# Kernel optimization log

Measured on AMD Instinct MI355X. Metric: run time of the kernel, lower is better.

The kernel has to match this reference:

```python
import jax, jax.numpy as jnp
import numpy as np

K_TOP = 4          # self.k
NUM_EXPERTS = 16   # self.num_experts
LOSS_COEF = 0.01


def setup_inputs() -> dict:
    key = jax.random.key(0)
    k0, k1, k2, k3, k4 = jax.random.split(key, 5)
    B, Cin, Cout, H, Wd, E = 16, 64, 64, 64, 64, NUM_EXPERTS
    x = jax.random.normal(k0, (B, Cin, H, Wd), dtype=jnp.float32)
    w_gate = jax.random.normal(k1, (Cin, E), dtype=jnp.float32) * 0.1
    w_noise = jax.random.normal(k2, (Cin, E), dtype=jnp.float32) * 0.1
    W = jax.random.normal(k3, (E, Cout, Cin, 3, 3), dtype=jnp.float32) * (1.0 / np.sqrt(Cin * 9).astype(np.float32))
    b = jax.random.normal(k4, (E, Cout), dtype=jnp.float32) * 0.01
    return {"x": x, "w_gate": w_gate, "w_noise": w_noise, "W": W, "b": b, "train": 0}


def _cv_squared(v):
    # torch .var() is unbiased (ddof=1)
    v = v.astype(jnp.float32)
    return jnp.var(v, ddof=1) / (jnp.mean(v) ** 2 + 1e-10)


def reference(x, w_gate, w_noise, W, b, train):
    B = x.shape[0]
    E = NUM_EXPERTS
    # gate_x = flatten(avgpool(x)) -> [B, Cin]
    gate_x = jnp.mean(x, axis=(2, 3))
    clean_logits = gate_x @ w_gate                      # [B, E]
    # train == 0 (eval): no noise branch; logits = softmax(clean_logits)
    logits = jax.nn.softmax(clean_logits, axis=1)
    top_vals, top_idx = jax.lax.top_k(logits, min(K_TOP + 1, E))
    tk_vals = top_vals[:, :K_TOP]                       # [B, k]
    tk_idx = top_idx[:, :K_TOP]                         # [B, k]
    tk_gates = tk_vals / (jnp.sum(tk_vals, axis=1, keepdims=True) + 1e-6)
    gates = jnp.zeros_like(logits).at[jnp.arange(B)[:, None], tk_idx].set(tk_gates)  # [B, E]
    # load (eval path): count of nonzero gates per expert
    load = jax.lax.stop_gradient(jnp.sum(gates > 0, axis=0)).astype(jnp.float32)     # [E]
    importance = jnp.sum(gates, axis=0)                 # [E]
    loss = (_cv_squared(importance) + _cv_squared(load)) * LOSS_COEF
    # dispatch/combine == dense gated mixture: zero-gate experts contribute 0.
    def conv_one(w):
        return jax.lax.conv_general_dilated(
            x, w, window_strides=(1, 1), padding=[(1, 1), (1, 1)],
            dimension_numbers=("NCHW", "OIHW", "NCHW"))
    expert_outs = jax.vmap(conv_one)(W) + b[:, None, :, None, None]  # [E, B, Cout, H, W]
    y = jnp.einsum("ebchw,be->bchw", expert_outs, gates)
    return (y, loss)
```

## Files before the change

### kernel.cpp

```cpp
#include <hip/hip_runtime.h>
#include <hip/hip_bf16.h>


typedef __attribute__((ext_vector_type(8))) short bf16x8;
typedef __attribute__((ext_vector_type(4))) float f32x4;

__device__ inline unsigned short f2bf(float f) {
  unsigned u = __builtin_bit_cast(unsigned, f);
  unsigned r = u + 0x7FFFu + ((u >> 16) & 1u);
  return (unsigned short)(r >> 16);
}

__global__ __launch_bounds__(256) void transpose_kernel(const float* __restrict__ x,
                                                        unsigned short* __restrict__ xt,
                                                        float* __restrict__ gpart) {
  int bh = blockIdx.x;
  int b = bh >> 6, h = bh & 63;
  __shared__ float tile[64][65];
  int t = threadIdx.x;
  int w = t & 63, c0 = t >> 6;
#pragma unroll
  for (int i = 0; i < 16; ++i) {
    int ci = c0 * 16 + i;
    tile[ci][w] = x[(((size_t)b * 64 + ci) * 64 + h) * 64 + w];
  }
  __syncthreads();
  if (t < 64) {
    float s = 0.f;
#pragma unroll
    for (int w2 = 0; w2 < 64; ++w2) s += tile[t][w2];
    gpart[(size_t)bh * 64 + t] = s;
  }
#pragma unroll
  for (int it = 0; it < 2; ++it) {
    int idx = t + it * 256;
    int g = idx >> 6;
    int wo = idx & 63;
    bf16x8 v;
#pragma unroll
    for (int j = 0; j < 8; ++j) v[j] = (short)f2bf(tile[g * 8 + j][wo]);
    *(bf16x8*)(xt + (((size_t)bh * 8 + g) * 64 + wo) * 8) = v;
  }
}

__global__ __launch_bounds__(256) void gate_kernel(const float* __restrict__ gpart,
                                                   const float* __restrict__ w_gate,
                                                   float* __restrict__ tkg,
                                                   int* __restrict__ tki,
                                                   float* __restrict__ loss_out) {
  __shared__ float red[4][64];
  __shared__ float sgx[16][64];
  __shared__ float sl[16][16];
  __shared__ float sg[16][16];
  __shared__ float simp[16], sld[16];
  int t = threadIdx.x;
  int hg = t >> 6, ci = t & 63;
  for (int b = 0; b < 16; ++b) {
    float s = 0.f;
#pragma unroll
    for (int hh = 0; hh < 16; ++hh)
      s += gpart[((size_t)(b * 64 + hg * 16 + hh)) * 64 + ci];
    red[hg][ci] = s;
    __syncthreads();
    if (t < 64) sgx[b][t] = (red[0][t] + red[1][t] + red[2][t] + red[3][t]) * (1.0f / 4096.0f);
    __syncthreads();
  }
  {
    int b = t >> 4, e = t & 15;
    float acc = 0.f;
    for (int c = 0; c < 64; ++c) acc += sgx[b][c] * w_gate[c * 16 + e];
    sl[b][e] = acc;
  }
  __syncthreads();
  if (t < 16) {
    int bb = t;
    float m = sl[bb][0];
#pragma unroll
    for (int i = 1; i < 16; ++i) m = fmaxf(m, sl[bb][i]);
    float p[16];
    float z = 0.f;
#pragma unroll
    for (int i = 0; i < 16; ++i) { p[i] = expf(sl[bb][i] - m); z += p[i]; }
#pragma unroll
    for (int i = 0; i < 16; ++i) p[i] /= z;
    int idx[4]; float val[4];
    bool used[16];
#pragma unroll
    for (int i = 0; i < 16; ++i) used[i] = false;
    for (int j = 0; j < 4; ++j) {
      int bi = 0; float bv = -1.f;
      for (int i = 0; i < 16; ++i)
        if (!used[i] && p[i] > bv) { bv = p[i]; bi = i; }
      used[bi] = true; idx[j] = bi; val[j] = bv;
    }
    float ssum = val[0] + val[1] + val[2] + val[3] + 1e-6f;
#pragma unroll
    for (int i = 0; i < 16; ++i) sg[bb][i] = 0.f;
    for (int j = 0; j < 4; ++j) {
      float g = val[j] / ssum;
      sg[bb][idx[j]] = g;
      tkg[bb * 4 + j] = g;
      tki[bb * 4 + j] = idx[j];
    }
  }
  __syncthreads();
  if (t < 16) {
    int ee = t; float imp = 0.f, ld = 0.f;
    for (int bb = 0; bb < 16; ++bb) {
      float g = sg[bb][ee];
      imp += g;
      if (g > 0.f) ld += 1.f;
    }
    simp[ee] = imp; sld[ee] = ld;
  }
  __syncthreads();
  if (t == 0) {
    float mi = 0.f, ml = 0.f;
    for (int i = 0; i < 16; ++i) { mi += simp[i]; ml += sld[i]; }
    mi *= (1.f / 16.f); ml *= (1.f / 16.f);
    float vi = 0.f, vl = 0.f;
    for (int i = 0; i < 16; ++i) {
      float d = simp[i] - mi; vi += d * d;
      float dl = sld[i] - ml; vl += dl * dl;
    }
    vi *= (1.f / 15.f); vl *= (1.f / 15.f);
    loss_out[0] = (vi / (mi * mi + 1e-10f) + vl / (ml * ml + 1e-10f)) * 0.01f;
  }
}

__global__ __launch_bounds__(256) void combine_kernel(const float* __restrict__ W,
                                                      const float* __restrict__ bias,
                                                      const float* __restrict__ tkg,
                                                      const int* __restrict__ tki,
                                                      unsigned short* __restrict__ wc,
                                                      float* __restrict__ bc) {
  int cog = blockIdx.x;
  int b = blockIdx.y;
  int t = threadIdx.x;
  __shared__ float g[4];
  __shared__ int e[4];
  __shared__ float was[2304];
  if (t < 4) { g[t] = tkg[b * 4 + t]; e[t] = tki[b * 4 + t]; }
  __syncthreads();
  float g0 = g[0], g1 = g[1], g2 = g[2], g3 = g[3];
  int e0 = e[0], e1 = e[1], e2 = e[2], e3 = e[3];
  if (cog == 0 && t < 64)
    bc[b * 64 + t] = g0 * bias[e0 * 64 + t] + g1 * bias[e1 * 64 + t] +
                     g2 * bias[e2 * 64 + t] + g3 * bias[e3 * 64 + t];
  const float* b0 = W + e0 * 36864 + cog * 2304;
  const float* b1 = W + e1 * 36864 + cog * 2304;
  const float* b2 = W + e2 * 36864 + cog * 2304;
  const float* b3 = W + e3 * 36864 + cog * 2304;
  float acc[9];
#pragma unroll
  for (int j = 0; j < 9; ++j) {
    int o = t + j * 256;
    acc[j] = g0 * b0[o] + g1 * b1[o] + g2 * b2[o] + g3 * b3[o];
  }
#pragma unroll
  for (int j = 0; j < 9; ++j) was[t + j * 256] = acc[j];
  __syncthreads();
  for (int v = t; v < 288; v += 256) {
    int co_l = v & 3, gg = (v >> 2) & 7, p = v >> 5;
    bf16x8 ov;
#pragma unroll
    for (int j = 0; j < 8; ++j)
      ov[j] = (short)f2bf(was[co_l * 576 + (gg * 8 + j) * 9 + p]);
    *(bf16x8*)(wc + (size_t)b * 36864 + ((p * 8 + gg) * 64 + cog * 4 + co_l) * 8) = ov;
  }
}

__global__ __launch_bounds__(512) void conv_mfma(const unsigned short* __restrict__ xt,
                                                 const unsigned short* __restrict__ wc,
                                                 const float* __restrict__ bc,
                                                 float* __restrict__ y) {
  int rt = blockIdx.x;
  int b = blockIdx.y;
  int tid = threadIdx.x;
  int wv = tid >> 6, L = tid & 63;
  int lane15 = L & 15, quad = L >> 4;
  int row = rt * 4 + (wv >> 1);
  int colbase = (wv & 1) * 32;
  const unsigned short* xtb = xt + ((size_t)b << 18);
  const unsigned short* wcb = wc + (size_t)b * 36864;
  f32x4 acc[4][2];
#pragma unroll
  for (int mt = 0; mt < 4; ++mt)
#pragma unroll
    for (int nt = 0; nt < 2; ++nt) acc[mt][nt] = (f32x4){0.f, 0.f, 0.f, 0.f};
  const bf16x8 zero = {0, 0, 0, 0, 0, 0, 0, 0};
#pragma unroll
  for (int p = 0; p < 9; ++p) {
    int dr = p / 3, dc = p % 3;
    int h = row + dr - 1;
    bool hok = (unsigned)h < 64u;
#pragma unroll
    for (int ck = 0; ck < 2; ++ck) {
      int g = ck * 4 + quad;
      bf16x8 bfr[2];
#pragma unroll
      for (int nt = 0; nt < 2; ++nt) {
        int w = colbase + nt * 16 + lane15 + dc - 1;
        bf16x8 v = zero;
        if (hok && (unsigned)w < 64u)
          v = *(const bf16x8*)(xtb + (((h << 3) + g) << 9) + (w << 3));
        bfr[nt] = v;
      }
      bf16x8 afr[4];
#pragma unroll
      for (int mt = 0; mt < 4; ++mt)
        afr[mt] = *(const bf16x8*)(wcb + ((((p << 3) + g) << 6) + mt * 16 + lane15) * 8);
#pragma unroll
      for (int mt = 0; mt < 4; ++mt)
#pragma unroll
        for (int nt = 0; nt < 2; ++nt)
          acc[mt][nt] = __builtin_amdgcn_mfma_f32_16x16x32_bf16(afr[mt], bfr[nt], acc[mt][nt], 0, 0, 0);
    }
  }
#pragma unroll
  for (int mt = 0; mt < 4; ++mt) {
#pragma unroll
    for (int r = 0; r < 4; ++r) {
      int co = mt * 16 + quad * 4 + r;
      float bias = bc[(b << 6) + co];
#pragma unroll
      for (int nt = 0; nt < 2; ++nt) {
        int w = colbase + nt * 16 + lane15;
        y[(((size_t)(b << 6) + co) << 12) + (row << 6) + w] = acc[mt][nt][r] + bias;
      }
    }
  }
}

extern "C" void kernel_launch(void* const* d_in, const int* in_sizes, int n_in,
                              void* d_out, int out_size, void* d_ws, size_t ws_size,
                              hipStream_t stream) {
  const float* x = (const float*)d_in[0];
  const float* w_gate = (const float*)d_in[1];
  const float* W = (const float*)d_in[3];
  const float* bias = (const float*)d_in[4];
  float* out = (float*)d_out;
  float* ws = (float*)d_ws;

  float* gpart = ws;
  float* tkg = ws + 65536;
  int* tki = (int*)(ws + 65600);
  float* bc = ws + 65664;
  unsigned short* wc = (unsigned short*)(ws + 66688);
  unsigned short* xt = (unsigned short*)(ws + 361600);

  transpose_kernel<<<1024, 256, 0, stream>>>(x, xt, gpart);
  gate_kernel<<<1, 256, 0, stream>>>(gpart, w_gate, tkg, tki, out + 4194304);
  {
    dim3 grid(16, 16);
    combine_kernel<<<grid, 256, 0, stream>>>(W, bias, tkg, tki, wc, bc);
  }
  {
    dim3 grid(16, 16);
    conv_mfma<<<grid, 512, 0, stream>>>(xt, wc, bc, out);
  }
}
```

Baseline: 113.8 us.

## Fuse gating into combine kernel and vectorize transpose loads

Removes the single-block gate kernel. Each combine block now recomputes its own batch's pooled features, logits, softmax and top-4, and one extra block column computes the loss. This drops a serialized one-block launch from the critical path at the cost of redundant gate computation across 16 blocks per batch. The transpose kernel also switches its input loads to float4 so each access is wider.

```diff
diff --git a/kernel.cpp b/kernel.cpp
--- a/kernel.cpp
+++ b/kernel.cpp
@@ -18,12 +18,19 @@
   int b = bh >> 6, h = bh & 63;
   __shared__ float tile[64][65];
   int t = threadIdx.x;
-  int w = t & 63, c0 = t >> 6;
-#pragma unroll
-  for (int i = 0; i < 16; ++i) {
-    int ci = c0 * 16 + i;
-    tile[ci][w] = x[(((size_t)b * 64 + ci) * 64 + h) * 64 + w];
-  }
+  const float4* xrow = (const float4*)(x + ((size_t)b * 64 * 64 + h) * 64) ;
+#pragma unroll
+  for (int k = 0; k < 4; ++k) {
+    int idx = t + k * 256;
+    int ci = idx >> 4;
+    int w4 = idx & 15;
+    float4 v = *(const float4*)(x + ((((size_t)b * 64 + ci) * 64 + h) * 64 + w4 * 4));
+    tile[ci][w4 * 4 + 0] = v.x;
+    tile[ci][w4 * 4 + 1] = v.y;
+    tile[ci][w4 * 4 + 2] = v.z;
+    tile[ci][w4 * 4 + 3] = v.w;
+  }
+  (void)xrow;
   __syncthreads();
   if (t < 64) {
     float s = 0.f;
@@ -43,104 +50,128 @@
   }
 }
 
-__global__ __launch_bounds__(256) void gate_kernel(const float* __restrict__ gpart,
-                                                   const float* __restrict__ w_gate,
-                                                   float* __restrict__ tkg,
-                                                   int* __restrict__ tki,
-                                                   float* __restrict__ loss_out) {
+__device__ inline void softmax_top4(const float* sl, float* gv, int* ge) {
+  float m = sl[0];
+#pragma unroll
+  for (int i = 1; i < 16; ++i) m = fmaxf(m, sl[i]);
+  float p[16];
+  float z = 0.f;
+#pragma unroll
+  for (int i = 0; i < 16; ++i) { p[i] = expf(sl[i] - m); z += p[i]; }
+#pragma unroll
+  for (int i = 0; i < 16; ++i) p[i] /= z;
+  bool used[16];
+#pragma unroll
+  for (int i = 0; i < 16; ++i) used[i] = false;
+  float val[4];
+  for (int j = 0; j < 4; ++j) {
+    int bi = 0; float bv = -1.f;
+    for (int i = 0; i < 16; ++i)
+      if (!used[i] && p[i] > bv) { bv = p[i]; bi = i; }
+    used[bi] = true; ge[j] = bi; val[j] = bv;
+  }
+  float ssum = val[0] + val[1] + val[2] + val[3] + 1e-6f;
+  for (int j = 0; j < 4; ++j) gv[j] = val[j] / ssum;
+}
+
+__global__ __launch_bounds__(256) void combine_gate_kernel(const float* __restrict__ gpart,
+                                                           const float* __restrict__ w_gate,
+                                                           const float* __restrict__ W,
+                                                           const float* __restrict__ bias,
+                                                           unsigned short* __restrict__ wc,
+                                                           float* __restrict__ bc,
+                                                           float* __restrict__ loss_out) {
+  int cog = blockIdx.x;
+  int b = blockIdx.y;
+  int t = threadIdx.x;
+
+  if (cog == 16) {
+    if (b != 0) return;
+    __shared__ float red[4][64];
+    __shared__ float sgx[16][64];
+    __shared__ float sl[16][16];
+    __shared__ float sg[16][16];
+    __shared__ float simp[16], sld[16];
+    int hg = t >> 6, ci = t & 63;
+    for (int bb = 0; bb < 16; ++bb) {
+      float s = 0.f;
+#pragma unroll
+      for (int hh = 0; hh < 16; ++hh)
+        s += gpart[((size_t)(bb * 64 + hg * 16 + hh)) * 64 + ci];
+      red[hg][ci] = s;
+      __syncthreads();
+      if (t < 64) sgx[bb][t] = (red[0][t] + red[1][t] + red[2][t] + red[3][t]) * (1.0f / 4096.0f);
+      __syncthreads();
+    }
+    {
+      int bb = t >> 4, e = t & 15;
+      float acc = 0.f;
+      for (int c = 0; c < 64; ++c) acc += sgx[bb][c] * w_gate[c * 16 + e];
+      sl[bb][e] = acc;
+    }
+    __syncthreads();
+    if (t < 16) {
+      float gv[4]; int ge[4];
+      softmax_top4(sl[t], gv, ge);
+#pragma unroll
+      for (int i = 0; i < 16; ++i) sg[t][i] = 0.f;
+      for (int j = 0; j < 4; ++j) sg[t][ge[j]] = gv[j];
+    }
+    __syncthreads();
+    if (t < 16) {
+      int ee = t; float imp = 0.f, ld = 0.f;
+      for (int bb = 0; bb < 16; ++bb) {
+        float g = sg[bb][ee];
+        imp += g;
+        if (g > 0.f) ld += 1.f;
+      }
+      simp[ee] = imp; sld[ee] = ld;
+    }
+    __syncthreads();
+    if (t == 0) {
+      float mi = 0.f, ml = 0.f;
+      for (int i = 0; i < 16; ++i) { mi += simp[i]; ml += sld[i]; }
+      mi *= (1.f / 16.f); ml *= (1.f / 16.f);
+      float vi = 0.f, vl = 0.f;
+      for (int i = 0; i < 16; ++i) {
+        float d = simp[i] - mi; vi += d * d;
+        float dl = sld[i] - ml; vl += dl * dl;
+      }
+      vi *= (1.f / 15.f); vl *= (1.f / 15.f);
+      loss_out[0] = (vi / (mi * mi + 1e-10f) + vl / (ml * ml + 1e-10f)) * 0.01f;
+    }
+    return;
+  }
+
   __shared__ float red[4][64];
-  __shared__ float sgx[16][64];
-  __shared__ float sl[16][16];
-  __shared__ float sg[16][16];
-  __shared__ float simp[16], sld[16];
-  int t = threadIdx.x;
-  int hg = t >> 6, ci = t & 63;
-  for (int b = 0; b < 16; ++b) {
+  __shared__ float sgx[64];
+  __shared__ float sl[16];
+  __shared__ float g[4];
+  __shared__ int e[4];
+  __shared__ float was[2304];
+  {
+    int hg = t >> 6, ci = t & 63;
     float s = 0.f;
 #pragma unroll
     for (int hh = 0; hh < 16; ++hh)
       s += gpart[((size_t)(b * 64 + hg * 16 + hh)) * 64 + ci];
     red[hg][ci] = s;
-    __syncthreads();
-    if (t < 64) sgx[b][t] = (red[0][t] + red[1][t] + red[2][t] + red[3][t]) * (1.0f / 4096.0f);
-    __syncthreads();
-  }
-  {
-    int b = t >> 4, e = t & 15;
+  }
+  __syncthreads();
+  if (t < 64) sgx[t] = (red[0][t] + red[1][t] + red[2][t] + red[3][t]) * (1.0f / 4096.0f);
+  __syncthreads();
+  if (t < 16) {
     float acc = 0.f;
-    for (int c = 0; c < 64; ++c) acc += sgx[b][c] * w_gate[c * 16 + e];
-    sl[b][e] = acc;
-  }
-  __syncthreads();
-  if (t < 16) {
-    int bb = t;
-    float m = sl[bb][0];
-#pragma unroll
-    for (int i = 1; i < 16; ++i) m = fmaxf(m, sl[bb][i]);
-    float p[16];
-    float z = 0.f;
-#pragma unroll
-    for (int i = 0; i < 16; ++i) { p[i] = expf(sl[bb][i] - m); z += p[i]; }
-#pragma unroll
-    for (int i = 0; i < 16; ++i) p[i] /= z;
-    int idx[4]; float val[4];
-    bool used[16];
-#pragma unroll
-    for (int i = 0; i < 16; ++i) used[i] = false;
-    for (int j = 0; j < 4; ++j) {
-      int bi = 0; float bv = -1.f;
-      for (int i = 0; i < 16; ++i)
-        if (!used[i] && p[i] > bv) { bv = p[i]; bi = i; }
-      used[bi] = true; idx[j] = bi; val[j] = bv;
-    }
-    float ssum = val[0] + val[1] + val[2] + val[3] + 1e-6f;
-#pragma unroll
-    for (int i = 0; i < 16; ++i) sg[bb][i] = 0.f;
-    for (int j = 0; j < 4; ++j) {
-      float g = val[j] / ssum;
-      sg[bb][idx[j]] = g;
-      tkg[bb * 4 + j] = g;
-      tki[bb * 4 + j] = idx[j];
-    }
-  }
-  __syncthreads();
-  if (t < 16) {
-    int ee = t; float imp = 0.f, ld = 0.f;
-    for (int bb = 0; bb < 16; ++bb) {
-      float g = sg[bb][ee];
-      imp += g;
-      if (g > 0.f) ld += 1.f;
-    }
-    simp[ee] = imp; sld[ee] = ld;
+    for (int c = 0; c < 64; ++c) acc += sgx[c] * w_gate[c * 16 + t];
+    sl[t] = acc;
   }
   __syncthreads();
   if (t == 0) {
-    float mi = 0.f, ml = 0.f;
-    for (int i = 0; i < 16; ++i) { mi += simp[i]; ml += sld[i]; }
-    mi *= (1.f / 16.f); ml *= (1.f / 16.f);
-    float vi = 0.f, vl = 0.f;
-    for (int i = 0; i < 16; ++i) {
-      float d = simp[i] - mi; vi += d * d;
-      float dl = sld[i] - ml; vl += dl * dl;
-    }
-    vi *= (1.f / 15.f); vl *= (1.f / 15.f);
-    loss_out[0] = (vi / (mi * mi + 1e-10f) + vl / (ml * ml + 1e-10f)) * 0.01f;
-  }
-}
-
-__global__ __launch_bounds__(256) void combine_kernel(const float* __restrict__ W,
-                                                      const float* __restrict__ bias,
-                                                      const float* __restrict__ tkg,
-                                                      const int* __restrict__ tki,
-                                                      unsigned short* __restrict__ wc,
-                                                      float* __restrict__ bc) {
-  int cog = blockIdx.x;
-  int b = blockIdx.y;
-  int t = threadIdx.x;
-  __shared__ float g[4];
-  __shared__ int e[4];
-  __shared__ float was[2304];
-  if (t < 4) { g[t] = tkg[b * 4 + t]; e[t] = tki[b * 4 + t]; }
+    float gv[4]; int ge[4];
+    softmax_top4(sl, gv, ge);
+#pragma unroll
+    for (int j = 0; j < 4; ++j) { g[j] = gv[j]; e[j] = ge[j]; }
+  }
   __syncthreads();
   float g0 = g[0], g1 = g[1], g2 = g[2], g3 = g[3];
   int e0 = e[0], e1 = e[1], e2 = e[2], e3 = e[3];
@@ -243,17 +274,15 @@
   float* ws = (float*)d_ws;
 
   float* gpart = ws;
-  float* tkg = ws + 65536;
-  int* tki = (int*)(ws + 65600);
-  float* bc = ws + 65664;
-  unsigned short* wc = (unsigned short*)(ws + 66688);
-  unsigned short* xt = (unsigned short*)(ws + 361600);
+  float* bc = ws + 65536;
+  unsigned short* wc = (unsigned short*)(ws + 66560);
+  unsigned short* xt = (unsigned short*)(ws + 361472);
 
   transpose_kernel<<<1024, 256, 0, stream>>>(x, xt, gpart);
-  gate_kernel<<<1, 256, 0, stream>>>(gpart, w_gate, tkg, tki, out + 4194304);
   {
-    dim3 grid(16, 16);
-    combine_kernel<<<grid, 256, 0, stream>>>(W, bias, tkg, tki, wc, bc);
+    dim3 grid(17, 16);
+    combine_gate_kernel<<<grid, 256, 0, stream>>>(gpart, w_gate, W, bias, wc, bc,
+                                                  out + 4194304);
   }
   {
     dim3 grid(16, 16);
```

New measurement: 106.8 us. 1.07x faster.
